# Kernel optimization log

Measured on AMD Instinct MI355X. Metric: run time of the kernel, lower is better.

The kernel has to match this reference:

```python
import jax, jax.numpy as jnp
import numpy as np

# Matcher __init__ weights (constants of the module)
COST_CLASS, COST_OBJECTNESS, COST_GIOU, COST_CENTER = 1.0, 0.0, 2.0, 0.0


def _lsa_minrows(cost):
    """Min-cost rectangular linear sum assignment (Jonker-Volgenant style,
    same algorithm/semantics as scipy.optimize.linear_sum_assignment).
    cost: [n, m] with n <= m. Returns col4row[n]: assigned column per row.
    Inner Dijkstra steps are vectorized over columns."""
    cost = np.asarray(cost, dtype=np.float64)
    n, m = cost.shape
    u = np.zeros(n)
    v = np.zeros(m)
    path = np.full(m, -1, dtype=np.int64)
    col4row = np.full(n, -1, dtype=np.int64)
    row4col = np.full(m, -1, dtype=np.int64)
    for cur_row in range(n):
        shortest = np.full(m, np.inf)
        SR = np.zeros(n, dtype=bool)
        SC = np.zeros(m, dtype=bool)
        remaining = np.arange(m)
        min_val = 0.0
        i = cur_row
        sink = -1
        while sink == -1:
            SR[i] = True
            # relax reduced costs of all unvisited columns at once
            r = min_val + cost[i, remaining] - u[i] - v[remaining]
            upd = r < shortest[remaining]
            cols = remaining[upd]
            path[cols] = i
            shortest[cols] = r[upd]
            k = int(np.argmin(shortest[remaining]))
            j = int(remaining[k])
            min_val = shortest[j]
            if row4col[j] == -1:
                sink = j
            else:
                i = int(row4col[j])
            SC[j] = True
            remaining = np.delete(remaining, k)
        # dual variable update
        u[cur_row] += min_val
        sr = SR.copy()
        sr[cur_row] = False
        rows = np.nonzero(sr)[0]
        u[rows] += min_val - shortest[col4row[rows]]
        cols = np.nonzero(SC)[0]
        v[cols] -= min_val - shortest[cols]
        # augment along the alternating path
        j = sink
        while True:
            i = int(path[j])
            row4col[j] = i
            col4row[i], j = j, col4row[i]
            if i == cur_row:
                break
    return col4row


def setup_inputs() -> dict:
    key = jax.random.key(0)
    ks = jax.random.split(key, 5)
    B, Q, G, C = 64, 256, 64, 768
    return {
        "last_sem_cls_scores": jax.random.normal(ks[0], (B, Q, C), dtype=jnp.float32),
        "gious": jax.random.uniform(ks[1], (B, Q, G), dtype=jnp.float32, minval=-1.0, maxval=1.0),
        "positive_map": jax.random.uniform(ks[2], (B, G, C), dtype=jnp.float32),
        "sem_cls_label": jax.random.randint(ks[3], (B, G), 0, C, dtype=jnp.int64),
        "nactual_gt": jax.random.randint(ks[4], (B,), 1, G + 1, dtype=jnp.int64),
    }


def reference(last_sem_cls_scores, gious, positive_map, sem_cls_label, nactual_gt):
    B, Q = last_sem_cls_scores.shape[0], last_sem_cls_scores.shape[1]
    # cost-matrix construction (device side in the original)
    pred_cls_prob = jax.nn.softmax(last_sem_cls_scores, axis=-1)       # [B,Q,C]
    # class_mat is built in the original forward but never enters final_cost
    class_mat = -jnp.einsum('bqc,bgc->bqg', pred_cls_prob, positive_map)  # [B,Q,G]
    del class_mat
    final_cost = COST_GIOU * (-gious)                                   # [B,Q,G]
    # host-side per-batch Hungarian assignment (as in the original scipy loop)
    cost_np = np.asarray(jax.device_get(final_cost), dtype=np.float64)
    nact = np.asarray(jax.device_get(nactual_gt))
    per_prop_gt_inds = np.zeros((B, Q), dtype=np.int64)
    proposal_matched_mask = np.zeros((B, Q), dtype=np.float32)
    for b in range(B):
        nb = int(nact[b])
        if nb > 0:
            # transpose so rows = GT (nb <= Q); same optimal pairs as scipy on [Q, nb]
            col4row = _lsa_minrows(cost_np[b, :, :nb].T)  # gt g -> proposal col4row[g]
            per_prop_gt_inds[b, col4row] = np.arange(nb)
            proposal_matched_mask[b, col4row] = 1.0
    return jnp.asarray(per_prop_gt_inds), jnp.asarray(proposal_matched_mask)
```

## Files before the change

### kernel.cpp

```cpp
#include <hip/hip_runtime.h>
#include <float.h>
#include <limits.h>

#define QN 256
#define GN 64

__device__ __forceinline__ double mkdbl(int lo, int hi) { return __hiloint2double(hi, lo); }

__device__ __forceinline__ void wave_argmin(double &val, int &idx) {
#define AM_STEP(CTRL, RMASK)                                                   \
  {                                                                            \
    int lo  = __double2loint(val), hi = __double2hiint(val);                   \
    int nlo = __builtin_amdgcn_update_dpp(lo,  lo,  CTRL, RMASK, 0xf, false);  \
    int nhi = __builtin_amdgcn_update_dpp(hi,  hi,  CTRL, RMASK, 0xf, false);  \
    int nix = __builtin_amdgcn_update_dpp(idx, idx, CTRL, RMASK, 0xf, false);  \
    double nv = mkdbl(nlo, nhi);                                               \
    bool take = (nv < val) || (nv == val && nix < idx);                        \
    val = take ? nv : val;                                                     \
    idx = take ? nix : idx;                                                    \
  }
  AM_STEP(0x111, 0xf)
  AM_STEP(0x112, 0xf)
  AM_STEP(0x114, 0xf)
  AM_STEP(0x118, 0xf)
  AM_STEP(0x142, 0xa)
  AM_STEP(0x143, 0xc)
#undef AM_STEP
  int lo = __builtin_amdgcn_readlane(__double2loint(val), 63);
  int hi = __builtin_amdgcn_readlane(__double2hiint(val), 63);
  idx    = __builtin_amdgcn_readlane(idx, 63);
  val    = mkdbl(lo, hi);
}

__global__ __launch_bounds__(64) void matcher_kernel(
    const float* __restrict__ gious,
    const int*   __restrict__ nactual,
    float*       __restrict__ out,
    int B)
{
  const int b = blockIdx.x;
  const int t = threadIdx.x;

  __shared__ float costQ[QN][GN + 1];
  __shared__ float costT[GN][QN];

  int nb = nactual[b];
  nb = nb < 0 ? 0 : (nb > GN ? GN : nb);

  const float4* gb4 = (const float4*)(gious + (size_t)b * QN * GN);
  {
    const int q_sub = t >> 4;
    const int g0    = 4 * (t & 15);
#pragma unroll 4
    for (int it = 0; it < 64; ++it) {
      float4 x = gb4[it * 64 + t];
      int q = it * 4 + q_sub;
      costQ[q][g0 + 0] = -2.0f * x.x;
      costQ[q][g0 + 1] = -2.0f * x.y;
      costQ[q][g0 + 2] = -2.0f * x.z;
      costQ[q][g0 + 3] = -2.0f * x.w;
    }
  }
  __syncthreads();
#pragma unroll
  for (int qq = 0; qq < 4; ++qq) {
    int q = qq * 64 + t;
#pragma unroll 8
    for (int g = 0; g < GN; ++g) costT[g][q] = costQ[q][g];
  }
  __syncthreads();

  double v0 = 0, v1 = 0, v2 = 0, v3 = 0;
  int r4c0 = -1, r4c1 = -1, r4c2 = -1, r4c3 = -1;
  double u = 0.0;
  int col4row = -1;

  const float* costRow0 = &costT[0][0];

  for (int cur = 0; cur < nb; ++cur) {
    double s0 = DBL_MAX, s1 = DBL_MAX, s2 = DBL_MAX, s3 = DBL_MAX;
    int p0 = -1, p1 = -1, p2 = -1, p3 = -1;
    int scm = 0;
    int sr  = 0;
    double min_val = 0.0;
    int i = cur;
    int sink = -1;

    while (sink < 0) {
      float4 c4 = *(const float4*)(costRow0 + i * QN + 4 * t);
      if (t == i) sr = 1;
      double u_i = mkdbl(__builtin_amdgcn_readlane(__double2loint(u), i),
                         __builtin_amdgcn_readlane(__double2hiint(u), i));
      double r;
      r = ((min_val + (double)c4.x) - u_i) - v0; if (!(scm & 1) && r < s0) { s0 = r; p0 = i; }
      r = ((min_val + (double)c4.y) - u_i) - v1; if (!(scm & 2) && r < s1) { s1 = r; p1 = i; }
      r = ((min_val + (double)c4.z) - u_i) - v2; if (!(scm & 4) && r < s2) { s2 = r; p2 = i; }
      r = ((min_val + (double)c4.w) - u_i) - v3; if (!(scm & 8) && r < s3) { s3 = r; p3 = i; }
      double bv = (scm & 1) ? DBL_MAX : s0;
      int    bj = (scm & 1) ? INT_MAX : 4 * t + 0;
      if (!(scm & 2) && s1 < bv) { bv = s1; bj = 4 * t + 1; }
      if (!(scm & 4) && s2 < bv) { bv = s2; bj = 4 * t + 2; }
      if (!(scm & 8) && s3 < bv) { bv = s3; bj = 4 * t + 3; }
      wave_argmin(bv, bj);
      min_val = bv;
      int jstar = bj;
      int jo = jstar >> 2, sl = jstar & 3;
      int rsel = (sl == 0) ? r4c0 : (sl == 1) ? r4c1 : (sl == 2) ? r4c2 : r4c3;
      int r4 = __builtin_amdgcn_readlane(rsel, jo);
      if (t == jo) scm |= (1 << sl);
      if (r4 < 0) sink = jstar;
      else        i = r4;
    }

    {
      int c  = col4row < 0 ? 0 : col4row;
      int ow = (c >> 2) & 63, sl2 = c & 3;
      double g0 = __shfl(s0, ow, 64);
      double g1 = __shfl(s1, ow, 64);
      double g2 = __shfl(s2, ow, 64);
      double g3 = __shfl(s3, ow, 64);
      double s_c = (sl2 == 0) ? g0 : (sl2 == 1) ? g1 : (sl2 == 2) ? g2 : g3;
      if (t == cur)  u += min_val;
      else if (sr)   u += min_val - s_c;
      if (scm & 1) v0 -= min_val - s0;
      if (scm & 2) v1 -= min_val - s1;
      if (scm & 4) v2 -= min_val - s2;
      if (scm & 8) v3 -= min_val - s3;
    }

    {
      int j = sink;
      while (true) {
        int jo = j >> 2, sl = j & 3;
        int pv = (sl == 0) ? p0 : (sl == 1) ? p1 : (sl == 2) ? p2 : p3;
        int pi = __builtin_amdgcn_readlane(pv, jo);
        if (t == jo) {
          if      (sl == 0) r4c0 = pi;
          else if (sl == 1) r4c1 = pi;
          else if (sl == 2) r4c2 = pi;
          else              r4c3 = pi;
        }
        int jn = __builtin_amdgcn_readlane(col4row, pi);
        if (t == pi) col4row = j;
        j = jn;
        if (pi == cur) break;
      }
    }
  }

  {
    const size_t BQ = (size_t)B * QN;
    int base = b * QN + 4 * t;
    float4 inds = make_float4(r4c0 >= 0 ? (float)r4c0 : 0.0f,
                              r4c1 >= 0 ? (float)r4c1 : 0.0f,
                              r4c2 >= 0 ? (float)r4c2 : 0.0f,
                              r4c3 >= 0 ? (float)r4c3 : 0.0f);
    float4 mask = make_float4(r4c0 >= 0 ? 1.0f : 0.0f,
                              r4c1 >= 0 ? 1.0f : 0.0f,
                              r4c2 >= 0 ? 1.0f : 0.0f,
                              r4c3 >= 0 ? 1.0f : 0.0f);
    *(float4*)&out[base]      = inds;
    *(float4*)&out[BQ + base] = mask;
  }
}

extern "C" void kernel_launch(void* const* d_in, const int* in_sizes, int n_in,
                              void* d_out, int out_size, void* d_ws, size_t ws_size,
                              hipStream_t stream) {
  const float* gious   = (const float*)d_in[1];
  const int*   nactual = (const int*)d_in[4];
  float*       out     = (float*)d_out;
  const int B = in_sizes[4];

  matcher_kernel<<<B, 64, 0, stream>>>(gious, nactual, out, B);
}
```

Baseline: 163.9 us.

## Keep cost columns in registers and split argmin into min plus ballot

Drops the two shared-memory cost arrays and the transpose stage. Each lane now holds its four proposal columns (64 GT values each) in register vectors, indexed by a wave-uniform row. The DPP argmin that carried an index is replaced by a value-only wave min, followed by a ballot and find-first to recover the lowest matching column. This removes the LDS staging and barriers and lightens the reduction, but needs 256 VGPRs for the cost data, which risks spills and lower occupancy (launch bounds pinned to one block).

Measured after the change: 320.0 us. 95.2% more time.

```diff
diff --git a/kernel.cpp b/kernel.cpp
--- a/kernel.cpp
+++ b/kernel.cpp
@@ -5,34 +5,32 @@
 #define QN 256
 #define GN 64
 
+typedef float fv64 __attribute__((ext_vector_type(64)));
+
 __device__ __forceinline__ double mkdbl(int lo, int hi) { return __hiloint2double(hi, lo); }
 
-__device__ __forceinline__ void wave_argmin(double &val, int &idx) {
-#define AM_STEP(CTRL, RMASK)                                                   \
-  {                                                                            \
-    int lo  = __double2loint(val), hi = __double2hiint(val);                   \
-    int nlo = __builtin_amdgcn_update_dpp(lo,  lo,  CTRL, RMASK, 0xf, false);  \
-    int nhi = __builtin_amdgcn_update_dpp(hi,  hi,  CTRL, RMASK, 0xf, false);  \
-    int nix = __builtin_amdgcn_update_dpp(idx, idx, CTRL, RMASK, 0xf, false);  \
-    double nv = mkdbl(nlo, nhi);                                               \
-    bool take = (nv < val) || (nv == val && nix < idx);                        \
-    val = take ? nv : val;                                                     \
-    idx = take ? nix : idx;                                                    \
+__device__ __forceinline__ double wave_min_f64(double mv) {
+#define MSTEP(CTRL, RMASK)                                                      \
+  {                                                                             \
+    int lo  = __double2loint(mv), hi = __double2hiint(mv);                      \
+    int nlo = __builtin_amdgcn_update_dpp(lo, lo, CTRL, RMASK, 0xf, false);     \
+    int nhi = __builtin_amdgcn_update_dpp(hi, hi, CTRL, RMASK, 0xf, false);     \
+    double nv = mkdbl(nlo, nhi);                                                \
+    mv = nv < mv ? nv : mv;                                                     \
   }
-  AM_STEP(0x111, 0xf)
-  AM_STEP(0x112, 0xf)
-  AM_STEP(0x114, 0xf)
-  AM_STEP(0x118, 0xf)
-  AM_STEP(0x142, 0xa)
-  AM_STEP(0x143, 0xc)
-#undef AM_STEP
-  int lo = __builtin_amdgcn_readlane(__double2loint(val), 63);
-  int hi = __builtin_amdgcn_readlane(__double2hiint(val), 63);
-  idx    = __builtin_amdgcn_readlane(idx, 63);
-  val    = mkdbl(lo, hi);
+  MSTEP(0x111, 0xf)
+  MSTEP(0x112, 0xf)
+  MSTEP(0x114, 0xf)
+  MSTEP(0x118, 0xf)
+  MSTEP(0x142, 0xa)
+  MSTEP(0x143, 0xc)
+#undef MSTEP
+  int lo = __builtin_amdgcn_readlane(__double2loint(mv), 63);
+  int hi = __builtin_amdgcn_readlane(__double2hiint(mv), 63);
+  return mkdbl(lo, hi);
 }
 
-__global__ __launch_bounds__(64) void matcher_kernel(
+__global__ __launch_bounds__(64, 1) void matcher_kernel(
     const float* __restrict__ gious,
     const int*   __restrict__ nactual,
     float*       __restrict__ out,
@@ -41,41 +39,35 @@
   const int b = blockIdx.x;
   const int t = threadIdx.x;
 
-  __shared__ float costQ[QN][GN + 1];
-  __shared__ float costT[GN][QN];
-
   int nb = nactual[b];
   nb = nb < 0 ? 0 : (nb > GN ? GN : nb);
 
-  const float4* gb4 = (const float4*)(gious + (size_t)b * QN * GN);
+  fv64 c0, c1, c2, c3;
   {
-    const int q_sub = t >> 4;
-    const int g0    = 4 * (t & 15);
-#pragma unroll 4
-    for (int it = 0; it < 64; ++it) {
-      float4 x = gb4[it * 64 + t];
-      int q = it * 4 + q_sub;
-      costQ[q][g0 + 0] = -2.0f * x.x;
-      costQ[q][g0 + 1] = -2.0f * x.y;
-      costQ[q][g0 + 2] = -2.0f * x.z;
-      costQ[q][g0 + 3] = -2.0f * x.w;
+    const float* gb = gious + (size_t)b * QN * GN;
+#define LOADK(K, CK)                                                            \
+    {                                                                           \
+      const float4* rp = (const float4*)(gb + (size_t)(4 * t + K) * GN);        \
+      _Pragma("unroll")                                                         \
+      for (int g4 = 0; g4 < 16; ++g4) {                                         \
+        float4 x = rp[g4];                                                      \
+        CK[4 * g4 + 0] = -2.0f * x.x;                                           \
+        CK[4 * g4 + 1] = -2.0f * x.y;                                           \
+        CK[4 * g4 + 2] = -2.0f * x.z;                                           \
+        CK[4 * g4 + 3] = -2.0f * x.w;                                           \
+      }                                                                         \
     }
+    LOADK(0, c0)
+    LOADK(1, c1)
+    LOADK(2, c2)
+    LOADK(3, c3)
+#undef LOADK
   }
-  __syncthreads();
-#pragma unroll
-  for (int qq = 0; qq < 4; ++qq) {
-    int q = qq * 64 + t;
-#pragma unroll 8
-    for (int g = 0; g < GN; ++g) costT[g][q] = costQ[q][g];
-  }
-  __syncthreads();
 
   double v0 = 0, v1 = 0, v2 = 0, v3 = 0;
   int r4c0 = -1, r4c1 = -1, r4c2 = -1, r4c3 = -1;
   double u = 0.0;
   int col4row = -1;
-
-  const float* costRow0 = &costT[0][0];
 
   for (int cur = 0; cur < nb; ++cur) {
     double s0 = DBL_MAX, s1 = DBL_MAX, s2 = DBL_MAX, s3 = DBL_MAX;
@@ -87,23 +79,33 @@
     int sink = -1;
 
     while (sink < 0) {
-      float4 c4 = *(const float4*)(costRow0 + i * QN + 4 * t);
-      if (t == i) sr = 1;
-      double u_i = mkdbl(__builtin_amdgcn_readlane(__double2loint(u), i),
-                         __builtin_amdgcn_readlane(__double2hiint(u), i));
+      int iu = __builtin_amdgcn_readfirstlane(i);
+      float cx = c0[iu], cy = c1[iu], cz = c2[iu], cw = c3[iu];
+      if (t == iu) sr = 1;
+      double u_i = mkdbl(__builtin_amdgcn_readlane(__double2loint(u), iu),
+                         __builtin_amdgcn_readlane(__double2hiint(u), iu));
       double r;
-      r = ((min_val + (double)c4.x) - u_i) - v0; if (!(scm & 1) && r < s0) { s0 = r; p0 = i; }
-      r = ((min_val + (double)c4.y) - u_i) - v1; if (!(scm & 2) && r < s1) { s1 = r; p1 = i; }
-      r = ((min_val + (double)c4.z) - u_i) - v2; if (!(scm & 4) && r < s2) { s2 = r; p2 = i; }
-      r = ((min_val + (double)c4.w) - u_i) - v3; if (!(scm & 8) && r < s3) { s3 = r; p3 = i; }
-      double bv = (scm & 1) ? DBL_MAX : s0;
-      int    bj = (scm & 1) ? INT_MAX : 4 * t + 0;
-      if (!(scm & 2) && s1 < bv) { bv = s1; bj = 4 * t + 1; }
-      if (!(scm & 4) && s2 < bv) { bv = s2; bj = 4 * t + 2; }
-      if (!(scm & 8) && s3 < bv) { bv = s3; bj = 4 * t + 3; }
-      wave_argmin(bv, bj);
-      min_val = bv;
-      int jstar = bj;
+      r = ((min_val + (double)cx) - u_i) - v0; if (!(scm & 1) && r < s0) { s0 = r; p0 = iu; }
+      r = ((min_val + (double)cy) - u_i) - v1; if (!(scm & 2) && r < s1) { s1 = r; p1 = iu; }
+      r = ((min_val + (double)cz) - u_i) - v2; if (!(scm & 4) && r < s2) { s2 = r; p2 = iu; }
+      r = ((min_val + (double)cw) - u_i) - v3; if (!(scm & 8) && r < s3) { s3 = r; p3 = iu; }
+      double sp0 = (scm & 1) ? DBL_MAX : s0;
+      double sp1 = (scm & 2) ? DBL_MAX : s1;
+      double sp2 = (scm & 4) ? DBL_MAX : s2;
+      double sp3 = (scm & 8) ? DBL_MAX : s3;
+      double m01 = sp1 < sp0 ? sp1 : sp0;
+      double m23 = sp3 < sp2 ? sp3 : sp2;
+      double mloc = m23 < m01 ? m23 : m01;
+      double mv = wave_min_f64(mloc);
+      int bj = INT_MAX;
+      if (sp3 == mv) bj = 4 * t + 3;
+      if (sp2 == mv) bj = 4 * t + 2;
+      if (sp1 == mv) bj = 4 * t + 1;
+      if (sp0 == mv) bj = 4 * t + 0;
+      unsigned long long ball = __ballot(bj != INT_MAX);
+      int fl = (int)__builtin_ctzll(ball);
+      int jstar = __builtin_amdgcn_readlane(bj, fl);
+      min_val = mv;
       int jo = jstar >> 2, sl = jstar & 3;
       int rsel = (sl == 0) ? r4c0 : (sl == 1) ? r4c1 : (sl == 2) ? r4c2 : r4c3;
       int r4 = __builtin_amdgcn_readlane(rsel, jo);
```
